# Performance work log

Hardware: AMD Instinct MI355X
Metric: run time of the kernel (lower is better)

## Reference

```python
import jax, jax.numpy as jnp
import numpy as np

N, LN, S, T = 50000, 64, 8, 4
E = 800000
MU = 0.9


def setup_inputs() -> dict:
    key = jax.random.key(0)
    ks = jax.random.split(key, 10)
    X_Node = jax.random.randint(ks[0], (E,), 0, N, dtype=jnp.int64) if jax.config.jax_enable_x64 else jax.random.randint(ks[0], (E,), 0, N).astype(jnp.int32)
    X_Neis = jax.random.randint(ks[1], (E,), 0, N).astype(X_Node.dtype)
    dg_list = jax.random.randint(ks[2], (E,), 1, 64).astype(jnp.float32)
    sc = 0.05
    W_emb = jax.random.normal(ks[3], (N, LN), jnp.float32) * sc
    Wxi = jax.random.normal(ks[4], (2 * LN, S * S), jnp.float32) * sc
    bxi = jnp.zeros((S * S,), jnp.float32)
    Wrou = jax.random.normal(ks[5], (LN, S), jnp.float32) * sc
    brou = jnp.zeros((S,), jnp.float32)
    Wout = jax.random.normal(ks[6], (LN + S, 3), jnp.float32) * sc
    bout = jnp.zeros((3,), jnp.float32)
    return {"X_Node": X_Node, "X_Neis": X_Neis, "dg_list": dg_list,
            "W_emb": W_emb, "Wxi": Wxi, "bxi": bxi,
            "Wrou": Wrou, "brou": brou, "Wout": Wout, "bout": bout}


def reference(X_Node, X_Neis, dg_list, W_emb, Wxi, bxi, Wrou, brou, Wout, bout):
    # Edge-wise feature gather: X = [emb[src] || emb[dst]]  -> [E, 2*LN]
    node_e = W_emb[X_Node]
    neis_e = W_emb[X_Neis]
    X = jnp.concatenate([node_e, neis_e], axis=1)
    # Hw precompute (loop-invariant): A [E,S,S], b [E,S]
    A = jnp.tanh(X @ Wxi + bxi).reshape(-1, S, S) * (MU / S) / dg_list[:, None, None]
    b = jnp.tanh(node_e @ Wrou + brou)

    states = jnp.zeros((N, S), dtype=W_emb.dtype)

    def step(states, _):
        H = states[X_Node]                      # gather [E, S]
        H = jnp.einsum('eij,ej->ei', A, H) + b  # per-edge small matvec
        # AggrSum's one-hot [V,E] matmul == scatter-add by X_Node
        new_states = jax.ops.segment_sum(H, X_Node, num_segments=N)
        return new_states, None

    states, _ = jax.lax.scan(step, states, None, length=T)
    logits = jnp.concatenate([W_emb, states], axis=1) @ Wout + bout
    return jax.nn.softmax(logits, axis=1)
```

## Files before the change

kernel.cpp:

```cpp
#include <hip/hip_runtime.h>
#include <hip/hip_fp16.h>
#include <math.h>

#define N_NODES 50000
#define LNDIM   64
#define E_EDGES 800000
#define MU_OVER_S 0.1125f
#define HPAD 16
#define NRANGE 8
#define RANGE_SZ ((N_NODES + NRANGE - 1) / NRANGE)
#define MAXDEG 48
#define BCAP 110000
#define BK_EPT 16
#define BK_EPB (256 * BK_EPT)
#define BK_NB ((E_EDGES + BK_EPB - 1) / BK_EPB)
#define GEMM_NB ((N_NODES + 63) / 64)
#define BV_TILES ((N_NODES + 255) / 256)
#define LOG2E 1.4426950408889634f

typedef _Float16 h2 __attribute__((ext_vector_type(2)));
typedef short    bf16x8 __attribute__((ext_vector_type(8)));
typedef float    f32x4  __attribute__((ext_vector_type(4)));

__device__ __forceinline__ unsigned short f2bf(float f) {
    unsigned int u = __float_as_uint(f);
    u = (u + 0x7FFFu + ((u >> 16) & 1u)) >> 16;
    return (unsigned short)u;
}
__device__ __forceinline__ h2 bits_h2(unsigned u) {
    union { unsigned x; h2 h; } c; c.x = u; return c.h;
}

__global__ __launch_bounds__(256) void prep_kernel(
    const float* __restrict__ Wxi, unsigned short* __restrict__ Bpk,
    int4* __restrict__ zp, int nz4)
{
    int gid = blockIdx.x * 256 + threadIdx.x;
    if (gid < 8192) {
        int jt = gid >> 10;
        int rem = gid & 1023;
        int h = rem >> 9;
        int rem2 = rem & 511;
        int l = rem2 >> 3, i = rem2 & 7;
        int k   = h * 32 + (l >> 4) * 8 + i;
        int row = (jt >= 4 ? 64 : 0) + k;
        int col = (jt & 3) * 16 + (l & 15);
        Bpk[gid] = f2bf(Wxi[row * 64 + col]);
    }
    if (gid < nz4) zp[gid] = make_int4(0, 0, 0, 0);
}

__global__ __launch_bounds__(256, 4) void fused_kernel(
    const float* __restrict__ W_emb, const float* __restrict__ bxi,
    const float* __restrict__ Wrou,  const float* __restrict__ brou,
    const float* __restrict__ Wout,
    const int* __restrict__ X_Node, const int* __restrict__ X_Neis,
    const float* __restrict__ dg_list,
    const unsigned short* __restrict__ Bpk,
    unsigned short* __restrict__ T1, unsigned short* __restrict__ U,
    float* __restrict__ Bv, float* __restrict__ EW,
    int* __restrict__ bkt_cursor, uint2* __restrict__ pairs)
{
    __shared__ int scnt[4][NRANGE];
    __shared__ int wpref[4][NRANGE];
    __shared__ int gbase[NRANGE];

    int tid = threadIdx.x;

    if (blockIdx.x < BK_NB) {
        int lane = tid & 63;
        int wid  = tid >> 6;
        int wavebase = blockIdx.x * BK_EPB + wid * (BK_EPT * 64);

        unsigned nd[BK_EPT], py[BK_EPT];
        int wcnt[NRANGE];
        #pragma unroll
        for (int r = 0; r < NRANGE; ++r) wcnt[r] = 0;

        #pragma unroll
        for (int i = 0; i < BK_EPT; ++i) {
            int e  = wavebase + i * 64 + lane;
            bool ok = e < E_EDGES;
            int ec = ok ? e : (E_EDGES - 1);
            int node = X_Node[ec];
            unsigned nei = (unsigned)X_Neis[ec];
            float sc = MU_OVER_S / dg_list[ec];
            __half_raw hr = __half_raw(__float2half(sc));
            py[i] = nei | ((unsigned)hr.x << 16);
            int r = ok ? (node / RANGE_SZ) : NRANGE;
            nd[i] = (unsigned)node | ((unsigned)r << 24);
            #pragma unroll
            for (int rr = 0; rr < NRANGE; ++rr)
                wcnt[rr] += __popcll(__ballot(r == rr));
        }

        if (lane < NRANGE) scnt[wid][lane] = wcnt[lane];
        __syncthreads();
        if (tid < NRANGE) {
            int c0 = scnt[0][tid], c1 = scnt[1][tid], c2 = scnt[2][tid], c3 = scnt[3][tid];
            wpref[0][tid] = 0;
            wpref[1][tid] = c0;
            wpref[2][tid] = c0 + c1;
            wpref[3][tid] = c0 + c1 + c2;
            gbase[tid] = atomicAdd(&bkt_cursor[tid * HPAD], c0 + c1 + c2 + c3);
        }
        __syncthreads();

        int wb[NRANGE];
        #pragma unroll
        for (int r = 0; r < NRANGE; ++r) wb[r] = gbase[r] + wpref[wid][r];

        #pragma unroll
        for (int i = 0; i < BK_EPT; ++i) {
            int r = nd[i] >> 24;
            #pragma unroll
            for (int rr = 0; rr < NRANGE; ++rr) {
                unsigned long long m = __ballot(r == rr);
                if (r == rr) {
                    int rank = __popcll(m & ((1ULL << lane) - 1ULL));
                    int pos  = wb[rr] + rank;
                    if (pos < BCAP)
                        pairs[(size_t)rr * BCAP + pos] =
                            make_uint2(nd[i] & 0xFFFFFFu, py[i]);
                }
                wb[rr] += __popcll(m);
            }
        }
        return;
    }

    if (blockIdx.x < BK_NB + GEMM_NB) {
        int gb   = blockIdx.x - BK_NB;
        int lane = tid & 63;
        int wid  = tid >> 6;
        int nodebase = gb * 64 + wid * 16;
        if (nodebase >= N_NODES) return;

        int r0 = lane & 15;
        int g  = lane >> 4;

        bf16x8 a[2];
        int arow = min(nodebase + r0, N_NODES - 1);
        const float* ap = W_emb + (size_t)arow * 64 + g * 8;
        #pragma unroll
        for (int h = 0; h < 2; ++h) {
            float4 q0 = *(const float4*)(ap + h * 32);
            float4 q1 = *(const float4*)(ap + h * 32 + 4);
            bf16x8 t;
            t[0] = (short)f2bf(q0.x); t[1] = (short)f2bf(q0.y);
            t[2] = (short)f2bf(q0.z); t[3] = (short)f2bf(q0.w);
            t[4] = (short)f2bf(q1.x); t[5] = (short)f2bf(q1.y);
            t[6] = (short)f2bf(q1.z); t[7] = (short)f2bf(q1.w);
            a[h] = t;
        }

        #pragma unroll
        for (int jt = 0; jt < 8; ++jt) {
            float binit = (jt < 4) ? bxi[(jt & 3) * 16 + r0] : 0.f;
            f32x4 acc;
            acc[0] = binit; acc[1] = binit; acc[2] = binit; acc[3] = binit;
            #pragma unroll
            for (int h = 0; h < 2; ++h) {
                bf16x8 b = *(const bf16x8*)(Bpk + ((size_t)(jt * 2 + h) * 64 + lane) * 8);
                acc = __builtin_amdgcn_mfma_f32_16x16x32_bf16(a[h], b, acc, 0, 0, 0);
            }
            unsigned short* outp = (jt < 4) ? T1 : U;
            int jcol = (jt & 3) * 16 + r0;
            #pragma unroll
            for (int r = 0; r < 4; ++r) {
                int node = nodebase + g * 4 + r;
                if (node < N_NODES) {
                    union { _Float16 h; unsigned short u; } cv;
                    cv.h = (_Float16)acc[r];
                    outp[(size_t)node * 64 + jcol] = cv.u;
                }
            }
        }
        return;
    }

    int bt = blockIdx.x - (BK_NB + GEMM_NB);
    int v  = bt * 256 + tid;
    if (v >= N_NODES) return;
    float acc[8], ew0 = 0.f, ew1 = 0.f, ew2 = 0.f;
    #pragma unroll
    for (int j = 0; j < 8; ++j) acc[j] = brou[j];
    const float* eb = W_emb + (size_t)v * 64;
    for (int kc = 0; kc < 4; ++kc) {
        float e16[16];
        const float4* er = (const float4*)(eb + kc * 16);
        #pragma unroll
        for (int t4 = 0; t4 < 4; ++t4) {
            float4 q = er[t4];
            e16[4*t4+0] = q.x; e16[4*t4+1] = q.y; e16[4*t4+2] = q.z; e16[4*t4+3] = q.w;
        }
        #pragma unroll
        for (int kk = 0; kk < 16; ++kk) {
            float ek = e16[kk];
            int   k  = kc * 16 + kk;
            const float* wr = Wrou + k * 8;
            #pragma unroll
            for (int j = 0; j < 8; ++j) acc[j] = fmaf(ek, wr[j], acc[j]);
            const float* wo = Wout + k * 3;
            ew0 = fmaf(ek, wo[0], ew0);
            ew1 = fmaf(ek, wo[1], ew1);
            ew2 = fmaf(ek, wo[2], ew2);
        }
    }
    float4* dst = (float4*)(Bv + (size_t)v * 8);
    dst[0] = make_float4(tanhf(acc[0]), tanhf(acc[1]), tanhf(acc[2]), tanhf(acc[3]));
    dst[1] = make_float4(tanhf(acc[4]), tanhf(acc[5]), tanhf(acc[6]), tanhf(acc[7]));
    *(float4*)(EW + (size_t)v * 4) = make_float4(ew0, ew1, ew2, 0.f);
}

__global__ __launch_bounds__(256) void scatter2_kernel(
    const uint2* __restrict__ pairs, const int* __restrict__ bkt_cursor,
    int* __restrict__ cnt_arr, unsigned* __restrict__ pk_s)
{
    int r = blockIdx.x & (NRANGE - 1);
    int i = (blockIdx.x >> 3) * 256 + threadIdx.x;
    if (i >= bkt_cursor[r * HPAD]) return;
    uint2 p = pairs[(size_t)r * BCAP + i];
    int pos = atomicAdd(&cnt_arr[(size_t)p.x * HPAD], 1);
    if (pos < MAXDEG) pk_s[(size_t)p.x * MAXDEG + pos] = p.y;
}

__global__ __launch_bounds__(256, 4) void main_kernel(
    const float* __restrict__ Wout, const float* __restrict__ bout,
    const unsigned short* __restrict__ T1, const unsigned short* __restrict__ U,
    const float* __restrict__ Bv, const float* __restrict__ EW,
    const int* __restrict__ cnt_arr, const unsigned* __restrict__ pk_s,
    float* __restrict__ out)
{
    int lane = threadIdx.x & 63;
    int wid  = threadIdx.x >> 6;
    int v    = blockIdx.x * 4 + wid;
    if (v >= N_NODES) return;

    int cntv = min(cnt_arr[(size_t)v * HPAD], MAXDEG);
    unsigned pkl = (lane < MAXDEG) ? pk_s[(size_t)v * MAXDEG + lane] : 0u;
    unsigned pk  = (lane < cntv) ? pkl : 0u;
    unsigned tu  = (unsigned)T1[(size_t)v * 64 + lane];
    h2 t2 = bits_h2(tu | (tu << 16));

    const h2 c1 = { (_Float16)0.13333334f,  (_Float16)0.13333334f };
    const h2 c0 = { (_Float16)-0.33333334f, (_Float16)-0.33333334f };

    float m0 = 0.f, m1 = 0.f;

    for (int k0 = 0; k0 < cntv; k0 += 16) {
        unsigned q[16], uu[16];
        #pragma unroll
        for (int x = 0; x < 16; ++x) {
            q[x]  = (unsigned)__builtin_amdgcn_readlane((int)pk, k0 + x);
            uu[x] = (unsigned)U[(size_t)(q[x] & 0xFFFFu) * 64 + lane];
        }
        __builtin_amdgcn_sched_barrier(0);
        #pragma unroll
        for (int p = 0; p < 8; ++p) {
            unsigned sc2 = (q[2*p] >> 16) | (q[2*p+1] & 0xFFFF0000u);
            h2 x   = bits_h2(uu[2*p] | (uu[2*p+1] << 16)) + t2;
            h2 x2  = x * x;
            h2 a   = x2 * c1 + c0;
            h2 th  = (x * x2) * a + x;
            if (p & 1) m1 = __builtin_amdgcn_fdot2(th, bits_h2(sc2), m1, false);
            else       m0 = __builtin_amdgcn_fdot2(th, bits_h2(sc2), m0, false);
        }
    }
    float macc = m0 + m1;

    int   j   = lane & 7;
    int   i   = lane >> 3;
    float cnt = (float)cntv;
    float cj  = cnt * Bv[v * 8 + j];
    float ci  = __shfl(cj, i);
    float sj  = cj;

    #pragma unroll
    for (int step = 0; step < 3; ++step) {
        float p = macc * sj;
        p += __shfl_xor(p, 1);
        p += __shfl_xor(p, 2);
        p += __shfl_xor(p, 4);
        float snew = p + ci;
        sj = __shfl(snew, j * 8);
    }

    float p0 = sj * Wout[(64 + j) * 3 + 0];
    float p1 = sj * Wout[(64 + j) * 3 + 1];
    float p2 = sj * Wout[(64 + j) * 3 + 2];
    #pragma unroll
    for (int m = 1; m < 8; m <<= 1) {
        p0 += __shfl_xor(p0, m);
        p1 += __shfl_xor(p1, m);
        p2 += __shfl_xor(p2, m);
    }
    float4 ewv = *(const float4*)(EW + (size_t)v * 4);
    float L0 = p0 + ewv.x + bout[0];
    float L1 = p1 + ewv.y + bout[1];
    float L2 = p2 + ewv.z + bout[2];
    float mx = fmaxf(L0, fmaxf(L1, L2));
    float e0 = __builtin_amdgcn_exp2f((L0 - mx) * LOG2E);
    float e1 = __builtin_amdgcn_exp2f((L1 - mx) * LOG2E);
    float e2 = __builtin_amdgcn_exp2f((L2 - mx) * LOG2E);
    float inv = __builtin_amdgcn_rcpf(e0 + e1 + e2);
    float rr = (lane == 0) ? e0 : (lane == 1 ? e1 : e2);
    if (lane < 3) out[v * 3 + lane] = rr * inv;
}

extern "C" void kernel_launch(void* const* d_in, const int* in_sizes, int n_in,
                              void* d_out, int out_size, void* d_ws, size_t ws_size,
                              hipStream_t stream)
{
    const int*   X_Node = (const int*)  d_in[0];
    const int*   X_Neis = (const int*)  d_in[1];
    const float* dg     = (const float*)d_in[2];
    const float* W_emb  = (const float*)d_in[3];
    const float* Wxi    = (const float*)d_in[4];
    const float* bxi    = (const float*)d_in[5];
    const float* Wrou   = (const float*)d_in[6];
    const float* brou   = (const float*)d_in[7];
    const float* Wout   = (const float*)d_in[8];
    const float* bout   = (const float*)d_in[9];
    float*       out    = (float*)d_out;

    char*  ws  = (char*)d_ws;
    size_t off = 0;
    auto alloc = [&](size_t bytes) -> void* {
        void* p = ws + off;
        off += (bytes + 255) & ~(size_t)255;
        return p;
    };
    unsigned short* T1      = (unsigned short*)alloc((size_t)N_NODES * 64 * 2);
    unsigned short* U       = (unsigned short*)alloc((size_t)N_NODES * 64 * 2);
    float*          Bv      = (float*)alloc((size_t)N_NODES * 8 * 4);
    float*          EW      = (float*)alloc((size_t)N_NODES * 4 * 4);
    int*            cnt_arr = (int*)  alloc((size_t)N_NODES * HPAD * 4);
    int*            bkt_cur = (int*)  alloc((size_t)NRANGE * HPAD * 4);
    uint2*          pairs   = (uint2*)alloc((size_t)NRANGE * BCAP * 8);
    unsigned*       pk_s    = (unsigned*)alloc(((size_t)N_NODES * MAXDEG + 64) * 4);
    unsigned short* Bpk     = (unsigned short*)alloc(8192 * 2);

    const int NZ4 = (N_NODES * HPAD + NRANGE * HPAD) / 4;

    prep_kernel<<<(NZ4 + 255) / 256, 256, 0, stream>>>(Wxi, Bpk, (int4*)cnt_arr, NZ4);
    fused_kernel<<<BK_NB + GEMM_NB + BV_TILES, 256, 0, stream>>>(
        W_emb, bxi, Wrou, brou, Wout, X_Node, X_Neis, dg, Bpk,
        T1, U, Bv, EW, bkt_cur, pairs);
    scatter2_kernel<<<((BCAP + 255) / 256) * NRANGE, 256, 0, stream>>>(
        pairs, bkt_cur, cnt_arr, pk_s);
    main_kernel<<<(N_NODES + 3) / 4, 256, 0, stream>>>(
        Wout, bout, T1, U, Bv, EW, cnt_arr, pk_s, out);
}
```

Before: 94.33 us.

## Restructure bucketing into per-block buckets and merge scatter with GEMM kernel

Replaces the global-atomic range buckets with fixed-capacity per-block, per-range buckets and per-block counts, so no global cursor atomic is needed. The zeroing of cnt_arr and the Wxi packing move into the bucketing kernel. The scatter pass is folded into the GEMM/Bv kernel, cutting the launch count from four to three and letting the scatter run concurrently with the GEMM blocks. The per-block capacity of 768 per range could overflow for skewed inputs, and many scatter blocks may be mostly idle.

```diff
diff --git a/kernel.cpp b/kernel.cpp
--- a/kernel.cpp
+++ b/kernel.cpp
@@ -10,10 +10,13 @@
 #define NRANGE 8
 #define RANGE_SZ ((N_NODES + NRANGE - 1) / NRANGE)
 #define MAXDEG 48
-#define BCAP 110000
 #define BK_EPT 16
 #define BK_EPB (256 * BK_EPT)
 #define BK_NB ((E_EDGES + BK_EPB - 1) / BK_EPB)
+#define BKCAP 768
+#define PACK_NB 32
+#define SC_SUB 3
+#define SC2_BLKS (BK_NB * SC_SUB * NRANGE)
 #define GEMM_NB ((N_NODES + 63) / 64)
 #define BV_TILES ((N_NODES + 255) / 256)
 #define LOG2E 1.4426950408889634f
@@ -31,106 +34,128 @@
     union { unsigned x; h2 h; } c; c.x = u; return c.h;
 }
 
-__global__ __launch_bounds__(256) void prep_kernel(
-    const float* __restrict__ Wxi, unsigned short* __restrict__ Bpk,
-    int4* __restrict__ zp, int nz4)
+__global__ __launch_bounds__(256, 4) void k1_kernel(
+    const int* __restrict__ X_Node, const int* __restrict__ X_Neis,
+    const float* __restrict__ dg_list, const float* __restrict__ Wxi,
+    int* __restrict__ cnt_arr, int* __restrict__ cntb,
+    uint2* __restrict__ pairs, unsigned short* __restrict__ Bpk)
 {
-    int gid = blockIdx.x * 256 + threadIdx.x;
-    if (gid < 8192) {
-        int jt = gid >> 10;
-        int rem = gid & 1023;
-        int h = rem >> 9;
-        int rem2 = rem & 511;
-        int l = rem2 >> 3, i = rem2 & 7;
-        int k   = h * 32 + (l >> 4) * 8 + i;
-        int row = (jt >= 4 ? 64 : 0) + k;
-        int col = (jt & 3) * 16 + (l & 15);
-        Bpk[gid] = f2bf(Wxi[row * 64 + col]);
-    }
-    if (gid < nz4) zp[gid] = make_int4(0, 0, 0, 0);
-}
-
-__global__ __launch_bounds__(256, 4) void fused_kernel(
+    int tid = threadIdx.x;
+
+    if (blockIdx.x >= BK_NB) {
+        int gid = (blockIdx.x - BK_NB) * 256 + tid;
+        if (gid < 8192) {
+            int jt = gid >> 10;
+            int rem = gid & 1023;
+            int h = rem >> 9;
+            int rem2 = rem & 511;
+            int l = rem2 >> 3, i = rem2 & 7;
+            int k   = h * 32 + (l >> 4) * 8 + i;
+            int row = (jt >= 4 ? 64 : 0) + k;
+            int col = (jt & 3) * 16 + (l & 15);
+            Bpk[gid] = f2bf(Wxi[row * 64 + col]);
+        }
+        return;
+    }
+
+    __shared__ int scnt[4][NRANGE];
+    __shared__ int wpref[4][NRANGE];
+
+    int b = blockIdx.x;
+    {
+        int4* cz = (int4*)cnt_arr;
+        const int n4 = N_NODES * HPAD / 4;
+        for (int i = b * 256 + tid; i < n4; i += BK_NB * 256)
+            cz[i] = make_int4(0, 0, 0, 0);
+    }
+
+    int lane = tid & 63;
+    int wid  = tid >> 6;
+    int wavebase = b * BK_EPB + wid * (BK_EPT * 64);
+
+    unsigned nd[BK_EPT], py[BK_EPT];
+    int wcnt[NRANGE];
+    #pragma unroll
+    for (int r = 0; r < NRANGE; ++r) wcnt[r] = 0;
+
+    #pragma unroll
+    for (int i = 0; i < BK_EPT; ++i) {
+        int e  = wavebase + i * 64 + lane;
+        bool ok = e < E_EDGES;
+        int ec = ok ? e : (E_EDGES - 1);
+        int node = X_Node[ec];
+        unsigned nei = (unsigned)X_Neis[ec];
+        float sc = MU_OVER_S / dg_list[ec];
+        __half_raw hr = __half_raw(__float2half(sc));
+        py[i] = nei | ((unsigned)hr.x << 16);
+        int r = ok ? (node / RANGE_SZ) : NRANGE;
+        nd[i] = (unsigned)node | ((unsigned)r << 24);
+        #pragma unroll
+        for (int rr = 0; rr < NRANGE; ++rr)
+            wcnt[rr] += __popcll(__ballot(r == rr));
+    }
+
+    if (lane < NRANGE) scnt[wid][lane] = wcnt[lane];
+    __syncthreads();
+    if (tid < NRANGE) {
+        int c0 = scnt[0][tid], c1 = scnt[1][tid], c2 = scnt[2][tid], c3 = scnt[3][tid];
+        wpref[0][tid] = 0;
+        wpref[1][tid] = c0;
+        wpref[2][tid] = c0 + c1;
+        wpref[3][tid] = c0 + c1 + c2;
+        cntb[tid * BK_NB + b] = c0 + c1 + c2 + c3;
+    }
+    __syncthreads();
+
+    int lwb[NRANGE];
+    #pragma unroll
+    for (int r = 0; r < NRANGE; ++r) lwb[r] = wpref[wid][r];
+
+    #pragma unroll
+    for (int i = 0; i < BK_EPT; ++i) {
+        int r = nd[i] >> 24;
+        #pragma unroll
+        for (int rr = 0; rr < NRANGE; ++rr) {
+            unsigned long long m = __ballot(r == rr);
+            if (r == rr) {
+                int rank = lwb[rr] + __popcll(m & ((1ULL << lane) - 1ULL));
+                if (rank < BKCAP)
+                    pairs[((size_t)(rr * BK_NB + b)) * BKCAP + rank] =
+                        make_uint2(nd[i] & 0xFFFFFFu, py[i]);
+            }
+            lwb[rr] += __popcll(m);
+        }
+    }
+}
+
+__global__ __launch_bounds__(256, 4) void k2_kernel(
     const float* __restrict__ W_emb, const float* __restrict__ bxi,
     const float* __restrict__ Wrou,  const float* __restrict__ brou,
     const float* __restrict__ Wout,
-    const int* __restrict__ X_Node, const int* __restrict__ X_Neis,
-    const float* __restrict__ dg_list,
+    const uint2* __restrict__ pairs, const int* __restrict__ cntb,
     const unsigned short* __restrict__ Bpk,
+    int* __restrict__ cnt_arr, unsigned* __restrict__ pk_s,
     unsigned short* __restrict__ T1, unsigned short* __restrict__ U,
-    float* __restrict__ Bv, float* __restrict__ EW,
-    int* __restrict__ bkt_cursor, uint2* __restrict__ pairs)
+    float* __restrict__ Bv, float* __restrict__ EW)
 {
-    __shared__ int scnt[4][NRANGE];
-    __shared__ int wpref[4][NRANGE];
-    __shared__ int gbase[NRANGE];
-
     int tid = threadIdx.x;
 
-    if (blockIdx.x < BK_NB) {
-        int lane = tid & 63;
-        int wid  = tid >> 6;
-        int wavebase = blockIdx.x * BK_EPB + wid * (BK_EPT * 64);
-
-        unsigned nd[BK_EPT], py[BK_EPT];
-        int wcnt[NRANGE];
-        #pragma unroll
-        for (int r = 0; r < NRANGE; ++r) wcnt[r] = 0;
-
-        #pragma unroll
-        for (int i = 0; i < BK_EPT; ++i) {
-            int e  = wavebase + i * 64 + lane;
-            bool ok = e < E_EDGES;
-            int ec = ok ? e : (E_EDGES - 1);
-            int node = X_Node[ec];
-            unsigned nei = (unsigned)X_Neis[ec];
-            float sc = MU_OVER_S / dg_list[ec];
-            __half_raw hr = __half_raw(__float2half(sc));
-            py[i] = nei | ((unsigned)hr.x << 16);
-            int r = ok ? (node / RANGE_SZ) : NRANGE;
-            nd[i] = (unsigned)node | ((unsigned)r << 24);
-            #pragma unroll
-            for (int rr = 0; rr < NRANGE; ++rr)
-                wcnt[rr] += __popcll(__ballot(r == rr));
-        }
-
-        if (lane < NRANGE) scnt[wid][lane] = wcnt[lane];
-        __syncthreads();
-        if (tid < NRANGE) {
-            int c0 = scnt[0][tid], c1 = scnt[1][tid], c2 = scnt[2][tid], c3 = scnt[3][tid];
-            wpref[0][tid] = 0;
-            wpref[1][tid] = c0;
-            wpref[2][tid] = c0 + c1;
-            wpref[3][tid] = c0 + c1 + c2;
-            gbase[tid] = atomicAdd(&bkt_cursor[tid * HPAD], c0 + c1 + c2 + c3);
-        }
-        __syncthreads();
-
-        int wb[NRANGE];
-        #pragma unroll
-        for (int r = 0; r < NRANGE; ++r) wb[r] = gbase[r] + wpref[wid][r];
-
-        #pragma unroll
-        for (int i = 0; i < BK_EPT; ++i) {
-            int r = nd[i] >> 24;
-            #pragma unroll
-            for (int rr = 0; rr < NRANGE; ++rr) {
-                unsigned long long m = __ballot(r == rr);
-                if (r == rr) {
-                    int rank = __popcll(m & ((1ULL << lane) - 1ULL));
-                    int pos  = wb[rr] + rank;
-                    if (pos < BCAP)
-                        pairs[(size_t)rr * BCAP + pos] =
-                            make_uint2(nd[i] & 0xFFFFFFu, py[i]);
-                }
-                wb[rr] += __popcll(m);
-            }
+    if (blockIdx.x < SC2_BLKS) {
+        int r = blockIdx.x & (NRANGE - 1);
+        int c = blockIdx.x >> 3;
+        int b = c / SC_SUB;
+        int s = c % SC_SUB;
+        int i = s * 256 + tid;
+        if (i < cntb[r * BK_NB + b]) {
+            uint2 p = pairs[((size_t)(r * BK_NB + b)) * BKCAP + i];
+            int pos = atomicAdd(&cnt_arr[(size_t)p.x * HPAD], 1);
+            if (pos < MAXDEG) pk_s[(size_t)p.x * MAXDEG + pos] = p.y;
         }
         return;
     }
 
-    if (blockIdx.x < BK_NB + GEMM_NB) {
-        int gb   = blockIdx.x - BK_NB;
+    if (blockIdx.x < SC2_BLKS + GEMM_NB) {
+        int gb   = blockIdx.x - SC2_BLKS;
         int lane = tid & 63;
         int wid  = tid >> 6;
         int nodebase = gb * 64 + wid * 16;
@@ -161,17 +186,17 @@
             acc[0] = binit; acc[1] = binit; acc[2] = binit; acc[3] = binit;
             #pragma unroll
             for (int h = 0; h < 2; ++h) {
-                bf16x8 b = *(const bf16x8*)(Bpk + ((size_t)(jt * 2 + h) * 64 + lane) * 8);
-                acc = __builtin_amdgcn_mfma_f32_16x16x32_bf16(a[h], b, acc, 0, 0, 0);
+                bf16x8 bfr = *(const bf16x8*)(Bpk + ((size_t)(jt * 2 + h) * 64 + lane) * 8);
+                acc = __builtin_amdgcn_mfma_f32_16x16x32_bf16(a[h], bfr, acc, 0, 0, 0);
             }
             unsigned short* outp = (jt < 4) ? T1 : U;
             int jcol = (jt & 3) * 16 + r0;
             #pragma unroll
-            for (int r = 0; r < 4; ++r) {
-                int node = nodebase + g * 4 + r;
+            for (int rr = 0; rr < 4; ++rr) {
+                int node = nodebase + g * 4 + rr;
                 if (node < N_NODES) {
                     union { _Float16 h; unsigned short u; } cv;
-                    cv.h = (_Float16)acc[r];
+                    cv.h = (_Float16)acc[rr];
                     outp[(size_t)node * 64 + jcol] = cv.u;
                 }
             }
@@ -179,7 +204,7 @@
         return;
     }
 
-    int bt = blockIdx.x - (BK_NB + GEMM_NB);
+    int bt = blockIdx.x - (SC2_BLKS + GEMM_NB);
     int v  = bt * 256 + tid;
     if (v >= N_NODES) return;
     float acc[8], ew0 = 0.f, ew1 = 0.f, ew2 = 0.f;
@@ -211,18 +236,6 @@
     dst[0] = make_float4(tanhf(acc[0]), tanhf(acc[1]), tanhf(acc[2]), tanhf(acc[3]));
     dst[1] = make_float4(tanhf(acc[4]), tanhf(acc[5]), tanhf(acc[6]), tanhf(acc[7]));
     *(float4*)(EW + (size_t)v * 4) = make_float4(ew0, ew1, ew2, 0.f);
-}
-
-__global__ __launch_bounds__(256) void scatter2_kernel(
-    const uint2* __restrict__ pairs, const int* __restrict__ bkt_cursor,
-    int* __restrict__ cnt_arr, unsigned* __restrict__ pk_s)
-{
-    int r = blockIdx.x & (NRANGE - 1);
-    int i = (blockIdx.x >> 3) * 256 + threadIdx.x;
-    if (i >= bkt_cursor[r * HPAD]) return;
-    uint2 p = pairs[(size_t)r * BCAP + i];
-    int pos = atomicAdd(&cnt_arr[(size_t)p.x * HPAD], 1);
-    if (pos < MAXDEG) pk_s[(size_t)p.x * MAXDEG + pos] = p.y;
 }
 
 __global__ __launch_bounds__(256, 4) void main_kernel(
@@ -336,19 +349,16 @@
     float*          Bv      = (float*)alloc((size_t)N_NODES * 8 * 4);
     float*          EW      = (float*)alloc((size_t)N_NODES * 4 * 4);
     int*            cnt_arr = (int*)  alloc((size_t)N_NODES * HPAD * 4);
-    int*            bkt_cur = (int*)  alloc((size_t)NRANGE * HPAD * 4);
-    uint2*          pairs   = (uint2*)alloc((size_t)NRANGE * BCAP * 8);
+    int*            cntb    = (int*)  alloc((size_t)NRANGE * BK_NB * 4);
+    uint2*          pairs   = (uint2*)alloc((size_t)NRANGE * BK_NB * BKCAP * 8);
     unsigned*       pk_s    = (unsigned*)alloc(((size_t)N_NODES * MAXDEG + 64) * 4);
     unsigned short* Bpk     = (unsigned short*)alloc(8192 * 2);
 
-    const int NZ4 = (N_NODES * HPAD + NRANGE * HPAD) / 4;
-
-    prep_kernel<<<(NZ4 + 255) / 256, 256, 0, stream>>>(Wxi, Bpk, (int4*)cnt_arr, NZ4);
-    fused_kernel<<<BK_NB + GEMM_NB + BV_TILES, 256, 0, stream>>>(
-        W_emb, bxi, Wrou, brou, Wout, X_Node, X_Neis, dg, Bpk,
-        T1, U, Bv, EW, bkt_cur, pairs);
-    scatter2_kernel<<<((BCAP + 255) / 256) * NRANGE, 256, 0, stream>>>(
-        pairs, bkt_cur, cnt_arr, pk_s);
+    k1_kernel<<<BK_NB + PACK_NB, 256, 0, stream>>>(
+        X_Node, X_Neis, dg, Wxi, cnt_arr, cntb, pairs, Bpk);
+    k2_kernel<<<SC2_BLKS + GEMM_NB + BV_TILES, 256, 0, stream>>>(
+        W_emb, bxi, Wrou, brou, Wout, pairs, cntb, Bpk,
+        cnt_arr, pk_s, T1, U, Bv, EW);
     main_kernel<<<(N_NODES + 3) / 4, 256, 0, stream>>>(
         Wout, bout, T1, U, Bv, EW, cnt_arr, pk_s, out);
 }
```

Result: no change. 94.54 us (+0.2%).
